# Optimization experiments

Hardware: AMD Instinct MI355X
Metric: run time of the kernel (lower is better)

Reference implementation:

```python
import jax, jax.numpy as jnp
import numpy as np

NUM_RBF = 16
TOP_K = 30
MAX_REL = 32  # max_relative_feature
EPS_D = 1e-6
LN_EPS = 1e-5


def _rbf(D):
    # D: [..., ] -> [..., NUM_RBF]
    mu = jnp.linspace(2.0, 22.0, NUM_RBF)
    sigma = (22.0 - 2.0) / NUM_RBF
    return jnp.exp(-(((D[..., None] - mu) / sigma) ** 2))


def _gather_nb(coords, E_idx):
    # coords: [B,L,3], E_idx: [B,L,K] -> [B,L,K,3]
    return jax.vmap(lambda c, i: c[i])(coords, E_idx)


def reference(X, mask, residue_idx, chain_labels, pe_w, pe_b, edge_w, ln_g, ln_b):
    B, L = X.shape[0], X.shape[1]
    N = X[:, :, 0, :]
    C = X[:, :, 1, :]
    Ca = X[:, :, 2, :]
    O = X[:, :, 3, :]
    # virtual C-beta
    b = Ca - N
    c = C - Ca
    a = jnp.cross(b, c)
    Cb = -0.58273431 * a + 0.56802827 * b - 0.54067466 * c + Ca

    # kNN over masked pairwise C-C distances
    mask2 = mask[:, None, :] * mask[:, :, None]  # [B,L,L]
    dX = C[:, None, :, :] - C[:, :, None, :]
    D = mask2 * jnp.sqrt(jnp.sum(dX ** 2, -1) + EPS_D)
    D_max = jnp.max(D, -1, keepdims=True)
    D_adjust = D + (1.0 - mask2) * D_max
    k = min(TOP_K, L)
    neg_vals, E_idx = jax.lax.top_k(-D_adjust, k)  # smallest distances
    D_neighbors = -neg_vals  # [B,L,K]

    # 25 RBF feature sets: first is the masked topk distance, then 24 atom pairs
    atoms = {'N': N, 'C': C, 'Ca': Ca, 'Cb': Cb, 'O': O}
    pairs = [('N','N'),('Ca','Ca'),('Cb','Cb'),('C','N'),('C','Ca'),('C','Cb'),
             ('N','Ca'),('N','Cb'),('Cb','Ca'),('N','C'),('Ca','C'),('Cb','C'),
             ('Ca','N'),('Cb','N'),('Ca','Cb'),('O','O'),('C','O'),('O','C'),
             ('N','O'),('O','N'),('Cb','O'),('O','Ca'),('O','Cb'),('Ca','O')]
    A_stack = jnp.stack([atoms[p[0]] for p in pairs], 0)  # [P,B,L,3]
    B_stack = jnp.stack([atoms[p[1]] for p in pairs], 0)  # [P,B,L,3]
    Bn = jax.vmap(lambda cb: _gather_nb(cb, E_idx))(B_stack)  # [P,B,L,K,3]
    D_pairs = jnp.sqrt(jnp.sum((A_stack[:, :, :, None, :] - Bn) ** 2, -1) + EPS_D)  # [P,B,L,K]
    RBF_pairs = _rbf(D_pairs)  # [P,B,L,K,R]
    P = len(pairs)
    RBF_pairs = jnp.moveaxis(RBF_pairs, 0, 3).reshape(B, L, k, P * NUM_RBF)
    RBF_all = jnp.concatenate([_rbf(D_neighbors), RBF_pairs], -1)  # [B,L,K,400]

    # positional encodings (relative residue offset gathered at neighbors)
    offset = residue_idx[:, :, None] - residue_idx[:, None, :]  # [B,L,L]
    offset = jnp.take_along_axis(offset, E_idx, axis=2)  # [B,L,K]
    d_chains = (chain_labels[:, :, None] - chain_labels[:, None, :] == 0).astype(jnp.int32)
    E_chains = jnp.take_along_axis(d_chains, E_idx, axis=2)  # [B,L,K]
    d = jnp.clip(offset + MAX_REL, 0, 2 * MAX_REL) * E_chains + (1 - E_chains) * (2 * MAX_REL + 1)
    E_positional = pe_w[d] + pe_b  # one-hot @ W == row gather; [B,L,K,16]

    E = jnp.concatenate([E_positional, RBF_all], -1)  # [B,L,K,416]
    E = E @ edge_w  # [B,L,K,128]
    mu = jnp.mean(E, -1, keepdims=True)
    var = jnp.mean((E - mu) ** 2, -1, keepdims=True)
    E = (E - mu) / jnp.sqrt(var + LN_EPS) * ln_g + ln_b
    return E, E_idx


def setup_inputs() -> dict:
    key = jax.random.key(0)
    ks = jax.random.split(key, 6)
    B, L = 4, 2048
    X = jax.random.normal(ks[0], (B, L, 4, 3), dtype=jnp.float32)
    mask = jnp.ones((B, L), dtype=jnp.float32)
    residue_idx = jnp.arange(B * L, dtype=jnp.int32).reshape(B, L)
    chain_labels = jnp.zeros((B, L), dtype=jnp.int32)
    pe_w = jax.random.normal(ks[1], (66, 16), dtype=jnp.float32) * 0.1
    pe_b = jax.random.normal(ks[2], (16,), dtype=jnp.float32) * 0.1
    edge_w = jax.random.normal(ks[3], (416, 128), dtype=jnp.float32) * 0.05
    ln_g = jnp.ones((128,), dtype=jnp.float32)
    ln_b = jnp.zeros((128,), dtype=jnp.float32)
    return {"X": X, "mask": mask, "residue_idx": residue_idx, "chain_labels": chain_labels,
            "pe_w": pe_w, "pe_b": pe_b, "edge_w": edge_w, "ln_g": ln_g, "ln_b": ln_b}
```

## Files before the change

### kernel.cpp

```cpp
#include <hip/hip_runtime.h>
#include <hip/hip_bf16.h>
#include <cstdint>
#include <cstddef>

#define Bc 4
#define Lc 2048
#define Kc 30
#define Fc 416
#define Nc 128

typedef __bf16 bf16x8 __attribute__((ext_vector_type(8)));
typedef float  f32x4  __attribute__((ext_vector_type(4)));
typedef unsigned short ushortx8 __attribute__((ext_vector_type(8)));

__constant__ int c_pa[24] = {0,2,3,1,1,1,0,0,3,0,2,3,2,3,2,4,1,4,0,4,3,4,4,2};
__constant__ int c_pb[24] = {0,2,3,0,2,3,2,3,2,1,1,1,0,0,3,4,4,1,4,0,4,2,3,2};

__device__ __forceinline__ unsigned long long u64min(unsigned long long a, unsigned long long b) {
    return a < b ? a : b;
}
__device__ __forceinline__ unsigned long long u64max(unsigned long long a, unsigned long long b) {
    return a > b ? a : b;
}

__device__ __forceinline__ unsigned short f2bf(float f) {
    __hip_bfloat16 h = __float2bfloat16(f);
    return *(unsigned short*)&h;
}

__device__ __forceinline__ void rbf8(float d, float mu0, float* v) {
    const float u0 = (d - mu0) * 0.8f;
    v[0] = __expf(-u0 * u0);
    float rr = __expf(fmaf(2.1333333f, u0, -1.1377778f));
    #pragma unroll
    for (int m = 1; m < 8; ++m) {
        v[m] = v[m - 1] * rr;
        rr *= 0.10274083f;
    }
}

template<int CTRL>
__device__ __forceinline__ float dpp_radd(float x) {
    const int r = __builtin_amdgcn_update_dpp(0, __float_as_int(x), CTRL, 0xf, 0xf, true);
    return x + __int_as_float(r);
}
__device__ __forceinline__ float row16_sum(float x) {
    x = dpp_radd<0x121>(x);
    x = dpp_radd<0x122>(x);
    x = dpp_radd<0x124>(x);
    x = dpp_radd<0x128>(x);
    return x;
}

__global__ __launch_bounds__(256) void prep_w(const float* __restrict__ Wg,
                                              unsigned short* __restrict__ Wt) {
    const int id = blockIdx.x * 256 + threadIdx.x;
    if (id < Fc * Nc) {
        const int n = id / Fc, k = id - n * Fc;
        Wt[id] = f2bf(Wg[k * Nc + n]);
    }
}

__global__ __launch_bounds__(512) void topk4(
    const float* __restrict__ X, const float* __restrict__ mask,
    int* __restrict__ eidx, float* __restrict__ dnb, float* __restrict__ outEidx)
{
#pragma clang fp contract(off)
    __shared__ float4 cp[Lc];
    __shared__ unsigned long long pairs[8][256];
    __shared__ int scnt[8];

    const int t = threadIdx.x;
    const int lane = t & 63, wv = t >> 6;
    const int row = blockIdx.x * 8 + wv;
    const int b   = blockIdx.x >> 8;

    #pragma unroll
    for (int s = 0; s < 4; ++s) {
        const int j = s * 512 + t;
        const float* p = X + (size_t)(b * Lc + j) * 12;
        float4 o;
        o.x = p[3]; o.y = p[4]; o.z = p[5];
        o.w = mask[b * Lc + j];
        cp[j] = o;
    }
    if (lane == 0) scnt[wv] = 0;
    __syncthreads();

    const float4 ci = cp[row & (Lc - 1)];
    const float cix = ci.x, ciy = ci.y, ciz = ci.z, mi = ci.w;

    float D[32], am[32];
    float dmax = -1e30f;
    #pragma unroll 8
    for (int s = 0; s < 32; ++s) {
        const float4 f4 = cp[s * 64 + lane];
        const float dx = f4.x - cix;
        const float dy = f4.y - ciy;
        const float dz = f4.z - ciz;
        const float ss = dx * dx + dy * dy + dz * dz;
        const float dist = sqrtf(ss + 1e-6f);
        const float m2 = mi * f4.w;
        D[s] = m2 * dist;
        am[s] = 1.0f - m2;
        dmax = fmaxf(dmax, D[s]);
    }
    #pragma unroll
    for (int off = 32; off; off >>= 1) dmax = fmaxf(dmax, __shfl_xor(dmax, off, 64));

    unsigned uv[32];
    unsigned long long lmin = ~0ULL;
    #pragma unroll 8
    for (int s = 0; s < 32; ++s) {
        const float Dadj = D[s] + am[s] * dmax;
        uv[s] = __float_as_uint(Dadj);
        const unsigned long long k =
            ((unsigned long long)uv[s] << 32) | (unsigned)(s * 64 + lane);
        lmin = u64min(lmin, k);
    }

    unsigned long long sv = lmin;
    #pragma unroll
    for (int k = 2; k <= 64; k <<= 1) {
        #pragma unroll
        for (int j = k >> 1; j > 0; j >>= 1) {
            const unsigned long long o =
                (unsigned long long)__shfl_xor((long long)sv, j, 64);
            const bool takeMin = (((lane & k) == 0) == ((lane & j) == 0));
            sv = takeMin ? u64min(sv, o) : u64max(sv, o);
        }
    }
    const unsigned long long Tkey =
        (unsigned long long)__shfl((long long)sv, 29, 64);

    #pragma unroll 8
    for (int s = 0; s < 32; ++s) {
        const unsigned long long key =
            ((unsigned long long)uv[s] << 32) | (unsigned)(s * 64 + lane);
        if (key <= Tkey) {
            const int pos = atomicAdd(&scnt[wv], 1);
            if (pos < 256) pairs[wv][pos] = key;
        }
    }
    const int S = min(scnt[wv], 256);

    for (int p = lane; p < S; p += 64) {
        const unsigned long long kp = pairs[wv][p];
        int r = 0;
        for (int q = 0; q < S; ++q)
            r += (pairs[wv][q] < kp) ? 1 : 0;
        if (r < Kc) {
            const int j = (int)(kp & 0xffffffffULL);
            eidx[row * Kc + r] = j;
            dnb[row * Kc + r] = __uint_as_float((unsigned)(kp >> 32));
            outEidx[(size_t)row * Kc + r] = (float)j;
        }
    }
}

__global__ __launch_bounds__(512, 4) void edge_mfma7(
    const float* __restrict__ X, const int* __restrict__ ridx, const int* __restrict__ clab,
    const float* __restrict__ pe_w, const float* __restrict__ pe_b,
    const unsigned short* __restrict__ Wt,
    const float* __restrict__ ln_g, const float* __restrict__ ln_b,
    const int* __restrict__ eidx, const float* __restrict__ dnb,
    float* __restrict__ outE)
{
    __shared__ unsigned short Bs[2][8][512];
    __shared__ float atomsA[8][17];
    __shared__ float atomsB[240][17];
    __shared__ float dnb_s[240];
    __shared__ int   pid_s[240];

    const int blk = blockIdx.x;
    const int t   = threadIdx.x;
    const int lane = t & 63, wv = t >> 6;
    const int b   = blk >> 8;
    const int cl  = lane & 15, q = lane >> 4;

    if (t < 248) {
        int j;
        float* dst;
        if (t < 240) {
            j = eidx[(blk * 8 + t / 30) * Kc + (t % 30)];
            dst = &atomsB[t][0];
            dnb_s[t] = dnb[(blk * 8 + t / 30) * Kc + (t % 30)];
            const int rowi = blk * 8 + t / 30;
            const int jg = b * Lc + j;
            const int off = ridx[rowi] - ridx[jg];
            const int ec  = (clab[rowi] == clab[jg]) ? 1 : 0;
            pid_s[t] = ec ? min(max(off + 32, 0), 64) : 65;
        } else {
            j = (blk * 8 + (t - 240)) & (Lc - 1);
            dst = &atomsA[t - 240][0];
        }
        const float* p = X + (size_t)(b * Lc + j) * 12;
        const float Nx = p[0],  Ny = p[1],  Nz = p[2];
        const float Cx = p[3],  Cy = p[4],  Cz = p[5];
        const float Cax = p[6], Cay = p[7], Caz = p[8];
        const float Ox = p[9],  Oy = p[10], Oz = p[11];
        const float bx = Cax - Nx, by = Cay - Ny, bz = Caz - Nz;
        const float cx = Cx - Cax, cy = Cy - Cay, cz = Cz - Caz;
        const float ax = by * cz - bz * cy;
        const float ay = bz * cx - bx * cz;
        const float az = bx * cy - by * cx;
        dst[0] = Nx;  dst[1] = Ny;  dst[2] = Nz;
        dst[3] = Cx;  dst[4] = Cy;  dst[5] = Cz;
        dst[6] = Cax; dst[7] = Cay; dst[8] = Caz;
        dst[9]  = -0.58273431f * ax + 0.56802827f * bx - 0.54067466f * cx + Cax;
        dst[10] = -0.58273431f * ay + 0.56802827f * by - 0.54067466f * cy + Cay;
        dst[11] = -0.58273431f * az + 0.56802827f * bz - 0.54067466f * cz + Caz;
        dst[12] = Ox; dst[13] = Oy; dst[14] = Oz;
    }

    const unsigned short* gW = Wt + (wv * 16 + cl) * Fc + q * 8;
    {
        *(ushortx8*)&Bs[0][wv][lane * 8] = *(const ushortx8*)gW;
    }
    __syncthreads();

    f32x4 acc[2][8];
    #pragma unroll
    for (int m = 0; m < 2; ++m)
        #pragma unroll
        for (int n = 0; n < 8; ++n) acc[m][n] = (f32x4){0.f, 0.f, 0.f, 0.f};

    const int row0 = wv * 32 + cl;
    const int row1 = row0 + 16;
    const int e0 = min(row0, 239), e1 = min(row1, 239);
    const int r0 = e0 / 30,        r1 = e1 / 30;

    auto afrag = [&](int kc, int e, int r) -> bf16x8 {
        float v[8];
        if (kc == 0) {
            if (q < 2) {
                const int base = pid_s[e] * 16 + q * 8;
                const float4 p0 = *(const float4*)&pe_w[base];
                const float4 p1 = *(const float4*)&pe_w[base + 4];
                const float4 b0 = *(const float4*)&pe_b[q * 8];
                const float4 b1 = *(const float4*)&pe_b[q * 8 + 4];
                v[0] = p0.x + b0.x; v[1] = p0.y + b0.y;
                v[2] = p0.z + b0.z; v[3] = p0.w + b0.w;
                v[4] = p1.x + b1.x; v[5] = p1.y + b1.y;
                v[6] = p1.z + b1.z; v[7] = p1.w + b1.w;
            } else {
                rbf8(dnb_s[e], (q == 2) ? 2.0f : 12.6666667f, v);
            }
        } else {
            const int p  = 2 * kc - 2 + (q >> 1);
            const int a_ = c_pa[p], b_ = c_pb[p];
            const float dx = atomsA[r][a_ * 3 + 0] - atomsB[e][b_ * 3 + 0];
            const float dy = atomsA[r][a_ * 3 + 1] - atomsB[e][b_ * 3 + 1];
            const float dz = atomsA[r][a_ * 3 + 2] - atomsB[e][b_ * 3 + 2];
            const float d = sqrtf(dx * dx + dy * dy + dz * dz + 1e-6f);
            rbf8(d, (q & 1) ? 12.6666667f : 2.0f, v);
        }
        ushortx8 o;
        #pragma unroll
        for (int m = 0; m < 8; ++m) o[m] = f2bf(v[m]);
        return __builtin_bit_cast(bf16x8, o);
    };

    bf16x8 a0c = afrag(0, e0, r0);
    bf16x8 a1c = afrag(0, e1, r1);

    for (int kc = 0; kc < 13; ++kc) {
        const int cur = kc & 1;
        ushortx8 st;
        bf16x8 a0n, a1n;
        if (kc < 12) {
            st = *(const ushortx8*)(gW + (kc + 1) * 32);
            a0n = afrag(kc + 1, e0, r0);
            a1n = afrag(kc + 1, e1, r1);
        }
        #pragma unroll
        for (int n = 0; n < 8; ++n) {
            const bf16x8 bb = __builtin_bit_cast(bf16x8,
                *(const ushortx8*)&Bs[cur][n][lane * 8]);
            acc[0][n] = __builtin_amdgcn_mfma_f32_16x16x32_bf16(a0c, bb, acc[0][n], 0, 0, 0);
            acc[1][n] = __builtin_amdgcn_mfma_f32_16x16x32_bf16(a1c, bb, acc[1][n], 0, 0, 0);
        }
        if (kc < 12) {
            *(ushortx8*)&Bs[cur ^ 1][wv][lane * 8] = st;
        }
        __syncthreads();
        a0c = a0n; a1c = a1n;
    }

    float gcol[8], bcol[8];
    #pragma unroll
    for (int n = 0; n < 8; ++n) {
        gcol[n] = ln_g[n * 16 + cl];
        bcol[n] = ln_b[n * 16 + cl];
    }
    #pragma unroll
    for (int m = 0; m < 2; ++m) {
        #pragma unroll
        for (int reg = 0; reg < 4; ++reg) {
            const int rl = wv * 32 + m * 16 + q * 4 + reg;
            float s1 = 0.f, s2 = 0.f;
            #pragma unroll
            for (int n = 0; n < 8; ++n) {
                const float v = acc[m][n][reg];
                s1 += v; s2 += v * v;
            }
            s1 = row16_sum(s1);
            s2 = row16_sum(s2);
            if (rl < 240) {
                const float mu = s1 * (1.0f / 128.0f);
                const float var = s2 * (1.0f / 128.0f) - mu * mu;
                const float rstd = rsqrtf(var + 1e-5f);
                const size_t base = ((size_t)(blk * 240 + rl)) * 128 + cl;
                #pragma unroll
                for (int n = 0; n < 8; ++n) {
                    outE[base + n * 16] =
                        (acc[m][n][reg] - mu) * rstd * gcol[n] + bcol[n];
                }
            }
        }
    }
}

extern "C" void kernel_launch(void* const* d_in, const int* in_sizes, int n_in,
                              void* d_out, int out_size, void* d_ws, size_t ws_size,
                              hipStream_t stream) {
    const float* X     = (const float*)d_in[0];
    const float* mask  = (const float*)d_in[1];
    const int*   ridx  = (const int*)d_in[2];
    const int*   clab  = (const int*)d_in[3];
    const float* pe_w  = (const float*)d_in[4];
    const float* pe_b  = (const float*)d_in[5];
    const float* edge_w = (const float*)d_in[6];
    const float* ln_g  = (const float*)d_in[7];
    const float* ln_b  = (const float*)d_in[8];

    float* outE   = (float*)d_out;
    float* outIdx = outE + (size_t)Bc * Lc * Kc * Nc;

    char* ws = (char*)d_ws;
    int*   eidx = (int*)ws;
    float* dnbw = (float*)(ws + 983040);
    unsigned short* Wt = (unsigned short*)(ws + 1966080);

    prep_w<<<208, 256, 0, stream>>>(edge_w, Wt);
    topk4<<<Bc * Lc / 8, 512, 0, stream>>>(X, mask, eidx, dnbw, outIdx);
    edge_mfma7<<<Bc * Lc / 8, 512, 0, stream>>>(X, ridx, clab, pe_w, pe_b, Wt,
                                                ln_g, ln_b, eidx, dnbw, outE);
}
```

Before: 93.06 us.

## Merge weight prep into topk launch and process two K-chunks per barrier

The separate weight-transpose kernel is folded into the top-k kernel as 104 extra blocks, which removes one kernel launch. The MFMA K-loop in the edge kernel now stages two 32-wide weight chunks per iteration with a doubled shared buffer, so the number of __syncthreads barriers drops from 13 to 7. The cost is more shared memory and more registers held live for the extra A fragments and prefetches, which could lower occupancy under the 512-thread, 4-block bound.

```diff
diff --git a/kernel.cpp b/kernel.cpp
--- a/kernel.cpp
+++ b/kernel.cpp
@@ -52,20 +52,19 @@
     return x;
 }
 
-__global__ __launch_bounds__(256) void prep_w(const float* __restrict__ Wg,
-                                              unsigned short* __restrict__ Wt) {
-    const int id = blockIdx.x * 256 + threadIdx.x;
-    if (id < Fc * Nc) {
-        const int n = id / Fc, k = id - n * Fc;
-        Wt[id] = f2bf(Wg[k * Nc + n]);
-    }
-}
-
-__global__ __launch_bounds__(512) void topk4(
+__global__ __launch_bounds__(512) void topk5(
     const float* __restrict__ X, const float* __restrict__ mask,
+    const float* __restrict__ Wg, unsigned short* __restrict__ Wt,
     int* __restrict__ eidx, float* __restrict__ dnb, float* __restrict__ outEidx)
 {
 #pragma clang fp contract(off)
+    if (blockIdx.x >= 1024) {
+        const int id = (blockIdx.x - 1024) * 512 + threadIdx.x;
+        const int n = id / Fc, k = id - n * Fc;
+        Wt[id] = f2bf(Wg[k * Nc + n]);
+        return;
+    }
+
     __shared__ float4 cp[Lc];
     __shared__ unsigned long long pairs[8][256];
     __shared__ int scnt[8];
@@ -158,7 +157,7 @@
     }
 }
 
-__global__ __launch_bounds__(512, 4) void edge_mfma7(
+__global__ __launch_bounds__(512, 4) void edge_mfma8(
     const float* __restrict__ X, const int* __restrict__ ridx, const int* __restrict__ clab,
     const float* __restrict__ pe_w, const float* __restrict__ pe_b,
     const unsigned short* __restrict__ Wt,
@@ -166,7 +165,7 @@
     const int* __restrict__ eidx, const float* __restrict__ dnb,
     float* __restrict__ outE)
 {
-    __shared__ unsigned short Bs[2][8][512];
+    __shared__ unsigned short Bs[2][2][8][512];
     __shared__ float atomsA[8][17];
     __shared__ float atomsB[240][17];
     __shared__ float dnb_s[240];
@@ -215,7 +214,8 @@
 
     const unsigned short* gW = Wt + (wv * 16 + cl) * Fc + q * 8;
     {
-        *(ushortx8*)&Bs[0][wv][lane * 8] = *(const ushortx8*)gW;
+        *(ushortx8*)&Bs[0][0][wv][lane * 8] = *(const ushortx8*)gW;
+        *(ushortx8*)&Bs[0][1][wv][lane * 8] = *(const ushortx8*)(gW + 32);
     }
     __syncthreads();
 
@@ -264,27 +264,47 @@
     bf16x8 a0c = afrag(0, e0, r0);
     bf16x8 a1c = afrag(0, e1, r1);
 
-    for (int kc = 0; kc < 13; ++kc) {
-        const int cur = kc & 1;
-        ushortx8 st;
+    for (int iv = 0; iv < 7; ++iv) {
+        const int cur = iv & 1;
+        const int kcA = 2 * iv;
+        const bool hasB = (kcA + 1) <= 12;
+        ushortx8 st0, st1;
+        if (iv < 6) {
+            st0 = *(const ushortx8*)(gW + (kcA + 2) * 32);
+            st1 = *(const ushortx8*)(gW + (kcA + 3) * 32);
+        }
         bf16x8 a0n, a1n;
-        if (kc < 12) {
-            st = *(const ushortx8*)(gW + (kc + 1) * 32);
-            a0n = afrag(kc + 1, e0, r0);
-            a1n = afrag(kc + 1, e1, r1);
+        if (hasB) {
+            a0n = afrag(kcA + 1, e0, r0);
+            a1n = afrag(kcA + 1, e1, r1);
         }
         #pragma unroll
         for (int n = 0; n < 8; ++n) {
             const bf16x8 bb = __builtin_bit_cast(bf16x8,
-                *(const ushortx8*)&Bs[cur][n][lane * 8]);
+                *(const ushortx8*)&Bs[cur][0][n][lane * 8]);
             acc[0][n] = __builtin_amdgcn_mfma_f32_16x16x32_bf16(a0c, bb, acc[0][n], 0, 0, 0);
             acc[1][n] = __builtin_amdgcn_mfma_f32_16x16x32_bf16(a1c, bb, acc[1][n], 0, 0, 0);
         }
-        if (kc < 12) {
-            *(ushortx8*)&Bs[cur ^ 1][wv][lane * 8] = st;
+        if (hasB) {
+            bf16x8 a0m, a1m;
+            if (iv < 6) {
+                a0m = afrag(kcA + 2, e0, r0);
+                a1m = afrag(kcA + 2, e1, r1);
+            }
+            #pragma unroll
+            for (int n = 0; n < 8; ++n) {
+                const bf16x8 bb = __builtin_bit_cast(bf16x8,
+                    *(const ushortx8*)&Bs[cur][1][n][lane * 8]);
+                acc[0][n] = __builtin_amdgcn_mfma_f32_16x16x32_bf16(a0n, bb, acc[0][n], 0, 0, 0);
+                acc[1][n] = __builtin_amdgcn_mfma_f32_16x16x32_bf16(a1n, bb, acc[1][n], 0, 0, 0);
+            }
+            a0c = a0m; a1c = a1m;
+        }
+        if (iv < 6) {
+            *(ushortx8*)&Bs[cur ^ 1][0][wv][lane * 8] = st0;
+            *(ushortx8*)&Bs[cur ^ 1][1][wv][lane * 8] = st1;
         }
         __syncthreads();
-        a0c = a0n; a1c = a1n;
     }
 
     float gcol[8], bcol[8];
@@ -342,8 +362,7 @@
     float* dnbw = (float*)(ws + 983040);
     unsigned short* Wt = (unsigned short*)(ws + 1966080);
 
-    prep_w<<<208, 256, 0, stream>>>(edge_w, Wt);
-    topk4<<<Bc * Lc / 8, 512, 0, stream>>>(X, mask, eidx, dnbw, outIdx);
-    edge_mfma7<<<Bc * Lc / 8, 512, 0, stream>>>(X, ridx, clab, pe_w, pe_b, Wt,
+    topk5<<<1024 + 104, 512, 0, stream>>>(X, mask, edge_w, Wt, eidx, dnbw, outIdx);
+    edge_mfma8<<<Bc * Lc / 8, 512, 0, stream>>>(X, ridx, clab, pe_w, pe_b, Wt,
                                                 ln_g, ln_b, eidx, dnbw, outE);
 }
```

Result: slower. 97.49 us (+4.8%).
